# Kernel optimization log

Measured on AMD Instinct MI355X. Metric: run time of the kernel, lower is better.

The kernel has to match this reference:

```python
import jax, jax.numpy as jnp
import numpy as np

B, T, I, H, L = 64, 512, 512, 512, 2

def _xavier(key, shape):
    fan_in, fan_out = shape
    limit = float(np.sqrt(6.0 / (fan_in + fan_out)))
    return jax.random.uniform(key, shape, jnp.float32, -limit, limit)

def setup_inputs() -> dict:
    key = jax.random.key(0)
    ks = jax.random.split(key, 16)
    x = jax.random.normal(ks[0], (B, T, I), jnp.float32)
    h = jax.random.normal(ks[1], (L, B, H), jnp.float32)
    c = jax.random.normal(ks[2], (L, B, H), jnp.float32)
    # Gate order: i, f, g, o (concatenated along output dim -> [*, 4H])
    W_x0 = jnp.concatenate([_xavier(ks[3 + j], (I, H)) for j in range(4)], axis=1)
    W_h0 = jnp.concatenate([_xavier(ks[7 + j], (H, H)) for j in range(4)], axis=1)
    W_x1 = jnp.concatenate([_xavier(ks[11], (H, H)), _xavier(ks[12], (H, H)),
                            _xavier(ks[13], (H, H)), _xavier(ks[14], (H, H))], axis=1)
    W_h1 = jnp.concatenate([jax.random.split(ks[15], 4)[j] is None or _xavier(jax.random.split(ks[15], 4)[j], (H, H)) for j in range(4)], axis=1)
    # 8 scalar biases per layer: (b_ii, b_hi, b_if, b_hf, b_ig, b_hg, b_io, b_ho); zero-init as in torch
    b0 = jnp.zeros((8,), jnp.float32)
    b1 = jnp.zeros((8,), jnp.float32)
    return {"x": x, "h": h, "c": c, "W_x0": W_x0, "W_h0": W_h0, "b0": b0,
            "W_x1": W_x1, "W_h1": W_h1, "b1": b1}

def _lstm_layer(xs, h0, c0, Wx, Wh, b):
    # xs: [B, T, D]; Wx: [D, 4H]; Wh: [H, 4H]; b: [8] scalars
    bg = b[0::2] + b[1::2]  # combined per-gate scalar biases [4]: i, f, g, o
    x_proj = jnp.einsum('btd,dk->btk', xs, Wx)  # precompute input GEMM: [B, T, 4H]

    def step(carry, xp_t):
        h, c = carry
        z = xp_t + h @ Wh  # [B, 4H]
        zi, zf, zg, zo = jnp.split(z, 4, axis=1)
        i = jax.nn.sigmoid(zi + bg[0])
        f = jax.nn.sigmoid(zf + bg[1])
        g = jnp.tanh(zg + bg[2])
        o = jax.nn.sigmoid(zo + bg[3])
        c_new = f * c + i * g
        h_new = o * jnp.tanh(c_new)
        return (h_new, c_new), h_new

    (hT, cT), ys = jax.lax.scan(step, (h0, c0), jnp.swapaxes(x_proj, 0, 1))
    return jnp.swapaxes(ys, 0, 1), hT, cT  # output [B, T, H]

def reference(x, h, c, W_x0, W_h0, b0, W_x1, W_h1, b1):
    out0, h0T, c0T = _lstm_layer(x, h[0], c[0], W_x0, W_h0, b0)
    out1, h1T, c1T = _lstm_layer(out0, h[1], c[1], W_x1, W_h1, b1)
    new_h = jnp.stack([h0T, h1T])  # [L, B, H]
    new_c = jnp.stack([c0T, c1T])
    return out1, new_h, new_c
```

## Files before the change

### kernel.cpp

```cpp
#include <hip/hip_runtime.h>
#include <hip/hip_bf16.h>

#define B_   64
#define T_   512
#define I_   512
#define H_   512
#define NBLK 128
#define NTHR 256

typedef short bf16x8 __attribute__((ext_vector_type(8)));
typedef float f32x4  __attribute__((ext_vector_type(4)));
typedef unsigned long long u64;
typedef unsigned short u16;

#define MFMA(a, b, c) __builtin_amdgcn_mfma_f32_16x16x32_bf16((a), (b), (c), 0, 0, 0)

__device__ __forceinline__ u16 f2b(float f) {
    __hip_bfloat16 h = __float2bfloat16(f);
    return __builtin_bit_cast(u16, h);
}

__device__ __forceinline__ bf16x8 coh_ld8(const u16* p) {
    u64 lo = __hip_atomic_load((const u64*)p,     __ATOMIC_RELAXED, __HIP_MEMORY_SCOPE_AGENT);
    u64 hi = __hip_atomic_load((const u64*)p + 1, __ATOMIC_RELAXED, __HIP_MEMORY_SCOPE_AGENT);
    union { u64 q[2]; bf16x8 v; } u;
    u.q[0] = lo; u.q[1] = hi;
    return u.v;
}

__device__ __forceinline__ bool flag_ge(const int* f, int idx, int tgt) {
    return __hip_atomic_load(f + idx, __ATOMIC_RELAXED, __HIP_MEMORY_SCOPE_AGENT) >= tgt;
}

__global__ void k_init(const float* __restrict__ x, const float* __restrict__ h,
                       u16* __restrict__ xb, u16* __restrict__ h0ring, u16* __restrict__ h1ring,
                       int* __restrict__ flags0, int* __restrict__ flags1) {
    long i = (long)blockIdx.x * 256 + threadIdx.x;
    if (i < 2097152) {
        const float* p = x + i * 8;
        float4 a = *(const float4*)p;
        float4 b = *(const float4*)(p + 4);
        union { u16 s[8]; bf16x8 v; } u;
        u.s[0]=f2b(a.x); u.s[1]=f2b(a.y); u.s[2]=f2b(a.z); u.s[3]=f2b(a.w);
        u.s[4]=f2b(b.x); u.s[5]=f2b(b.y); u.s[6]=f2b(b.z); u.s[7]=f2b(b.w);
        *(bf16x8*)(xb + i * 8) = u.v;
    } else if (i < 2097152 + 8192) {
        long j = i - 2097152;
        const float* p = h + j * 8;
        #pragma unroll
        for (int jj = 0; jj < 8; ++jj) {
            long idx = j * 8 + jj;
            u16 v = f2b(p[jj]);
            if (idx < 32768) h0ring[7 * 32768 + idx] = v;
            else             h1ring[7 * 32768 + (idx - 32768)] = v;
        }
    } else if (i < 2097152 + 8192 + 512) {
        int j = (int)(i - (2097152 + 8192));
        if (j < 256) flags0[j] = 0; else flags1[j - 256] = 0;
    }
}

__global__ __launch_bounds__(NTHR, 1) void k_lstm(
    const u16* __restrict__ xb,
    const float* __restrict__ Wx0, const float* __restrict__ Wh0, const float* __restrict__ b0,
    const float* __restrict__ Wx1, const float* __restrict__ Wh1, const float* __restrict__ b1,
    const float* __restrict__ c_in,
    u16* __restrict__ h0ring, u16* __restrict__ h1ring,
    int* __restrict__ flags0, int* __restrict__ flags1,
    float* __restrict__ cs,
    float* __restrict__ out)
{
    const int tid  = threadIdx.x;
    const int bid  = blockIdx.x;
    const int lay  = bid >> 6;
    const int g    = (bid >> 4) & 3;
    const int u    = bid & 15;
    const int wave = tid >> 6;
    const int lane = tid & 63;
    const int n    = lane & 15;
    const int quad = lane >> 4;
    const int R0   = g * 16;
    const int U0   = u * 32;

    __shared__ __align__(16) u16   hstage[2][16][520];
    __shared__ __align__(16) u16   sc_hb[4][16][8];
    __shared__ __align__(16) float sc_h [4][16][8];

    const float* Wx = lay ? Wx1 : Wx0;
    const float* Wh = lay ? Wh1 : Wh0;
    const float* bb = lay ? b1  : b0;
    const float bi = bb[0] + bb[1];
    const float bf = bb[2] + bb[3];
    const float bg = bb[4] + bb[5];
    const float bo = bb[6] + bb[7];

    bf16x8 breg[2][32];
    #pragma unroll
    for (int ct = 0; ct < 2; ++ct) {
        const int gate = ct * 2 + (n >> 3);
        const int gcol = gate * 512 + U0 + wave * 8 + (n & 7);
        #pragma unroll
        for (int f = 0; f < 32; ++f) {
            const int kbase = f * 32 + quad * 8;
            bf16x8 w;
            #pragma unroll
            for (int j = 0; j < 8; ++j) {
                const int k = kbase + j;
                const float v = (k < 512) ? Wx[(size_t)k * 2048 + gcol]
                                          : Wh[(size_t)(k - 512) * 2048 + gcol];
                w[j] = (short)f2b(v);
            }
            breg[ct][f] = w;
        }
    }

    int* myflag = (lay ? flags1 : flags0) + g * 16 + u;
    const int fidx = g * 16 + n;
    (void)cs;

    float creg[4];
    if (n < 8) {
        #pragma unroll
        for (int r = 0; r < 4; ++r)
            creg[r] = c_in[(size_t)lay * 32768
                           + (size_t)(R0 + quad * 4 + r) * 512 + U0 + wave * 8 + n];
    }

    const int sr  = tid & 15;
    const int sch = tid >> 4;

    for (int t = 0; t < 512; ++t) {
        f32x4 acc0 = {0.f, 0.f, 0.f, 0.f};
        f32x4 acc1 = {0.f, 0.f, 0.f, 0.f};

        if (lay == 0) {
            const u16* px = xb + ((size_t)(R0 + n) * T_ + t) * I_;
            bf16x8 xa[16];
            #pragma unroll
            for (int f = 0; f < 16; ++f) xa[f] = *(const bf16x8*)(px + f * 32 + quad * 8);
            #pragma unroll
            for (int f = 0; f < 16; ++f) {
                acc0 = MFMA(xa[f], breg[0][f], acc0);
                acc1 = MFMA(xa[f], breg[1][f], acc1);
            }
            const bool bp = (t & 3) == 0;
            for (;;) {
                bool ok = flag_ge(flags0, fidx, t);
                if (bp) ok = ok && flag_ge(flags1, fidx, t - 4);
                if (__all(ok)) break;
                __builtin_amdgcn_s_sleep(1);
            }
            asm volatile("" ::: "memory");
            const u16* src = h0ring + (size_t)((t - 1) & 7) * 32768
                             + (size_t)(R0 + sr) * 512 + sch * 32;
            bf16x8 v0 = coh_ld8(src);
            bf16x8 v1 = coh_ld8(src + 8);
            bf16x8 v2 = coh_ld8(src + 16);
            bf16x8 v3 = coh_ld8(src + 24);
            *(bf16x8*)&hstage[0][sr][sch * 32]      = v0;
            *(bf16x8*)&hstage[0][sr][sch * 32 + 8]  = v1;
            *(bf16x8*)&hstage[0][sr][sch * 32 + 16] = v2;
            *(bf16x8*)&hstage[0][sr][sch * 32 + 24] = v3;
            __syncthreads();
            #pragma unroll
            for (int f = 0; f < 16; ++f) {
                bf16x8 ha = *(const bf16x8*)&hstage[0][n][f * 32 + quad * 8];
                acc0 = MFMA(ha, breg[0][16 + f], acc0);
                acc1 = MFMA(ha, breg[1][16 + f], acc1);
            }
        } else {
            for (;;) {
                bool ok = flag_ge(flags1, fidx, t) && flag_ge(flags0, fidx, t + 1);
                if (__all(ok)) break;
                __builtin_amdgcn_s_sleep(1);
            }
            asm volatile("" ::: "memory");
            const u16* s0 = h0ring + (size_t)(t & 7) * 32768
                            + (size_t)(R0 + sr) * 512 + sch * 32;
            const u16* s1 = h1ring + (size_t)((t - 1) & 7) * 32768
                            + (size_t)(R0 + sr) * 512 + sch * 32;
            bf16x8 a0 = coh_ld8(s0);
            bf16x8 a1 = coh_ld8(s0 + 8);
            bf16x8 a2 = coh_ld8(s0 + 16);
            bf16x8 a3 = coh_ld8(s0 + 24);
            bf16x8 b0v = coh_ld8(s1);
            bf16x8 b1v = coh_ld8(s1 + 8);
            bf16x8 b2v = coh_ld8(s1 + 16);
            bf16x8 b3v = coh_ld8(s1 + 24);
            *(bf16x8*)&hstage[0][sr][sch * 32]      = a0;
            *(bf16x8*)&hstage[0][sr][sch * 32 + 8]  = a1;
            *(bf16x8*)&hstage[0][sr][sch * 32 + 16] = a2;
            *(bf16x8*)&hstage[0][sr][sch * 32 + 24] = a3;
            *(bf16x8*)&hstage[1][sr][sch * 32]      = b0v;
            *(bf16x8*)&hstage[1][sr][sch * 32 + 8]  = b1v;
            *(bf16x8*)&hstage[1][sr][sch * 32 + 16] = b2v;
            *(bf16x8*)&hstage[1][sr][sch * 32 + 24] = b3v;
            __syncthreads();
            #pragma unroll
            for (int f = 0; f < 16; ++f) {
                bf16x8 ha = *(const bf16x8*)&hstage[0][n][f * 32 + quad * 8];
                acc0 = MFMA(ha, breg[0][f], acc0);
                acc1 = MFMA(ha, breg[1][f], acc1);
            }
            #pragma unroll
            for (int f = 0; f < 16; ++f) {
                bf16x8 ha = *(const bf16x8*)&hstage[1][n][f * 32 + quad * 8];
                acc0 = MFMA(ha, breg[0][16 + f], acc0);
                acc1 = MFMA(ha, breg[1][16 + f], acc1);
            }
        }

        f32x4 x0, x1;
        #pragma unroll
        for (int r = 0; r < 4; ++r) {
            x0[r] = __shfl_xor(acc0[r], 8);
            x1[r] = __shfl_xor(acc1[r], 8);
        }
        if (n < 8) {
            #pragma unroll
            for (int r = 0; r < 4; ++r) {
                const int row = quad * 4 + r;
                const float zi = acc0[r] + bi;
                const float zf = x0[r]   + bf;
                const float zg = acc1[r] + bg;
                const float zo = x1[r]   + bo;
                const float ig = 1.f / (1.f + __expf(-zi));
                const float fg = 1.f / (1.f + __expf(-zf));
                const float gg = tanhf(zg);
                const float og = 1.f / (1.f + __expf(-zo));
                const float cn = fg * creg[r] + ig * gg;
                const float hn = og * tanhf(cn);
                creg[r] = cn;
                sc_hb[wave][row][n] = f2b(hn);
                sc_h [wave][row][n] = hn;
            }
        }
        asm volatile("s_waitcnt lgkmcnt(0)" ::: "memory");

        if (lane < 16) {
            const u64* s = (const u64*)&sc_hb[wave][lane][0];
            u64 q0 = s[0], q1 = s[1];
            u64* d = (u64*)((lay ? h1ring : h0ring) + (size_t)(t & 7) * 32768
                            + (size_t)(R0 + lane) * 512 + U0 + wave * 8);
            __hip_atomic_store(d,     q0, __ATOMIC_RELAXED, __HIP_MEMORY_SCOPE_AGENT);
            __hip_atomic_store(d + 1, q1, __ATOMIC_RELAXED, __HIP_MEMORY_SCOPE_AGENT);
        }
        asm volatile("s_waitcnt vmcnt(0)" ::: "memory");
        __syncthreads();
        if (tid == 0)
            __hip_atomic_store(myflag, t + 1, __ATOMIC_RELAXED, __HIP_MEMORY_SCOPE_AGENT);

        if (lay && lane < 16) {
            const float* s = &sc_h[wave][lane][0];
            f32x4 a  = *(const f32x4*)s;
            f32x4 b2 = *(const f32x4*)(s + 4);
            float* po = out + ((size_t)(R0 + lane) * T_ + t) * H_ + U0 + wave * 8;
            *(f32x4*)po       = a;
            *(f32x4*)(po + 4) = b2;
        }
        if (t == 511 && n < 8) {
            const size_t o1 = (size_t)B_ * T_ * H_;
            #pragma unroll
            for (int r = 0; r < 4; ++r) {
                const int grow = R0 + quad * 4 + r;
                out[o1 +         (size_t)lay * 32768 + (size_t)grow * 512 + U0 + wave * 8 + n]
                    = sc_h[wave][quad * 4 + r][n];
                out[o1 + 65536 + (size_t)lay * 32768 + (size_t)grow * 512 + U0 + wave * 8 + n]
                    = creg[r];
            }
        }
    }
}

extern "C" void kernel_launch(void* const* d_in, const int* in_sizes, int n_in,
                              void* d_out, int out_size, void* d_ws, size_t ws_size,
                              hipStream_t stream) {
    const float* x   = (const float*)d_in[0];
    const float* h   = (const float*)d_in[1];
    const float* c   = (const float*)d_in[2];
    const float* Wx0 = (const float*)d_in[3];
    const float* Wh0 = (const float*)d_in[4];
    const float* b0  = (const float*)d_in[5];
    const float* Wx1 = (const float*)d_in[6];
    const float* Wh1 = (const float*)d_in[7];
    const float* b1  = (const float*)d_in[8];
    float* out = (float*)d_out;

    u16* xb     = (u16*)d_ws;
    u16* h0ring = xb + 16777216;
    u16* h1ring = h0ring + 262144;
    int* flags0 = (int*)(h1ring + 262144);
    int* flags1 = flags0 + 256;
    float* cs   = (float*)(flags1 + 256);

    k_init<<<8226, 256, 0, stream>>>(x, h, xb, h0ring, h1ring, flags0, flags1);
    k_lstm<<<NBLK, NTHR, 0, stream>>>(xb, Wx0, Wh0, b0, Wx1, Wh1, b1, c,
                                      h0ring, h1ring, flags0, flags1, cs, out);
}
```

Before: 3.588 ms.

## Coalesce h ring loads, swizzle LDS staging, and single-wave publish of h

Replaces the per-thread 4x16-byte strided loads of the previous hidden state with fully coalesced 8-byte atomic loads, where consecutive threads read consecutive words of a row. The data is stored into an XOR-swizzled LDS layout to avoid bank conflicts. The layer-1 loops interleave the two h sources. The h writeback is restructured so wave 0 alone stores the whole 16x32 tile contiguously and then raises the flag, which drops one barrier-wait path but serialises publishing onto one wave.

```diff
diff --git a/kernel.cpp b/kernel.cpp
--- a/kernel.cpp
+++ b/kernel.cpp
@@ -20,12 +20,11 @@
     return __builtin_bit_cast(u16, h);
 }
 
-__device__ __forceinline__ bf16x8 coh_ld8(const u16* p) {
-    u64 lo = __hip_atomic_load((const u64*)p,     __ATOMIC_RELAXED, __HIP_MEMORY_SCOPE_AGENT);
-    u64 hi = __hip_atomic_load((const u64*)p + 1, __ATOMIC_RELAXED, __HIP_MEMORY_SCOPE_AGENT);
-    union { u64 q[2]; bf16x8 v; } u;
-    u.q[0] = lo; u.q[1] = hi;
-    return u.v;
+__device__ __forceinline__ u64 coh_ld64(const void* p) {
+    return __hip_atomic_load((const u64*)p, __ATOMIC_RELAXED, __HIP_MEMORY_SCOPE_AGENT);
+}
+__device__ __forceinline__ void coh_st64(void* p, u64 v) {
+    __hip_atomic_store((u64*)p, v, __ATOMIC_RELAXED, __HIP_MEMORY_SCOPE_AGENT);
 }
 
 __device__ __forceinline__ bool flag_ge(const int* f, int idx, int tgt) {
@@ -82,8 +81,8 @@
     const int R0   = g * 16;
     const int U0   = u * 32;
 
-    __shared__ __align__(16) u16   hstage[2][16][520];
-    __shared__ __align__(16) u16   sc_hb[4][16][8];
+    __shared__ __align__(16) u16   hstage[2][8192];
+    __shared__ __align__(16) u16   sc_all[16 * 36];
     __shared__ __align__(16) float sc_h [4][16][8];
 
     const float* Wx = lay ? Wx1 : Wx0;
@@ -126,9 +125,6 @@
                            + (size_t)(R0 + quad * 4 + r) * 512 + U0 + wave * 8 + n];
     }
 
-    const int sr  = tid & 15;
-    const int sch = tid >> 4;
-
     for (int t = 0; t < 512; ++t) {
         f32x4 acc0 = {0.f, 0.f, 0.f, 0.f};
         f32x4 acc1 = {0.f, 0.f, 0.f, 0.f};
@@ -151,20 +147,26 @@
                 __builtin_amdgcn_s_sleep(1);
             }
             asm volatile("" ::: "memory");
-            const u16* src = h0ring + (size_t)((t - 1) & 7) * 32768
-                             + (size_t)(R0 + sr) * 512 + sch * 32;
-            bf16x8 v0 = coh_ld8(src);
-            bf16x8 v1 = coh_ld8(src + 8);
-            bf16x8 v2 = coh_ld8(src + 16);
-            bf16x8 v3 = coh_ld8(src + 24);
-            *(bf16x8*)&hstage[0][sr][sch * 32]      = v0;
-            *(bf16x8*)&hstage[0][sr][sch * 32 + 8]  = v1;
-            *(bf16x8*)&hstage[0][sr][sch * 32 + 16] = v2;
-            *(bf16x8*)&hstage[0][sr][sch * 32 + 24] = v3;
+            const u16* base = h0ring + (size_t)((t - 1) & 7) * 32768;
+            u64 v[8];
+            #pragma unroll
+            for (int i = 0; i < 8; ++i) {
+                const int s = i * 256 + tid;
+                const int r = s >> 7, m = s & 127;
+                v[i] = coh_ld64(base + (size_t)(R0 + r) * 512 + m * 4);
+            }
+            #pragma unroll
+            for (int i = 0; i < 8; ++i) {
+                const int s = i * 256 + tid;
+                const int r = s >> 7, m = s & 127;
+                const int uu = m >> 1, sub = m & 1;
+                *(u64*)&hstage[0][r * 512 + (((uu ^ (r & 7)) << 3) | (sub << 2))] = v[i];
+            }
             __syncthreads();
             #pragma unroll
             for (int f = 0; f < 16; ++f) {
-                bf16x8 ha = *(const bf16x8*)&hstage[0][n][f * 32 + quad * 8];
+                bf16x8 ha = *(const bf16x8*)
+                    &hstage[0][n * 512 + (((f * 4 + quad) ^ (n & 7)) << 3)];
                 acc0 = MFMA(ha, breg[0][16 + f], acc0);
                 acc1 = MFMA(ha, breg[1][16 + f], acc1);
             }
@@ -175,38 +177,35 @@
                 __builtin_amdgcn_s_sleep(1);
             }
             asm volatile("" ::: "memory");
-            const u16* s0 = h0ring + (size_t)(t & 7) * 32768
-                            + (size_t)(R0 + sr) * 512 + sch * 32;
-            const u16* s1 = h1ring + (size_t)((t - 1) & 7) * 32768
-                            + (size_t)(R0 + sr) * 512 + sch * 32;
-            bf16x8 a0 = coh_ld8(s0);
-            bf16x8 a1 = coh_ld8(s0 + 8);
-            bf16x8 a2 = coh_ld8(s0 + 16);
-            bf16x8 a3 = coh_ld8(s0 + 24);
-            bf16x8 b0v = coh_ld8(s1);
-            bf16x8 b1v = coh_ld8(s1 + 8);
-            bf16x8 b2v = coh_ld8(s1 + 16);
-            bf16x8 b3v = coh_ld8(s1 + 24);
-            *(bf16x8*)&hstage[0][sr][sch * 32]      = a0;
-            *(bf16x8*)&hstage[0][sr][sch * 32 + 8]  = a1;
-            *(bf16x8*)&hstage[0][sr][sch * 32 + 16] = a2;
-            *(bf16x8*)&hstage[0][sr][sch * 32 + 24] = a3;
-            *(bf16x8*)&hstage[1][sr][sch * 32]      = b0v;
-            *(bf16x8*)&hstage[1][sr][sch * 32 + 8]  = b1v;
-            *(bf16x8*)&hstage[1][sr][sch * 32 + 16] = b2v;
-            *(bf16x8*)&hstage[1][sr][sch * 32 + 24] = b3v;
+            const u16* base0 = h0ring + (size_t)(t & 7) * 32768;
+            const u16* base1 = h1ring + (size_t)((t - 1) & 7) * 32768;
+            u64 v0[8], v1[8];
+            #pragma unroll
+            for (int i = 0; i < 8; ++i) {
+                const int s = i * 256 + tid;
+                const int r = s >> 7, m = s & 127;
+                v0[i] = coh_ld64(base0 + (size_t)(R0 + r) * 512 + m * 4);
+                v1[i] = coh_ld64(base1 + (size_t)(R0 + r) * 512 + m * 4);
+            }
+            #pragma unroll
+            for (int i = 0; i < 8; ++i) {
+                const int s = i * 256 + tid;
+                const int r = s >> 7, m = s & 127;
+                const int uu = m >> 1, sub = m & 1;
+                const int off = r * 512 + (((uu ^ (r & 7)) << 3) | (sub << 2));
+                *(u64*)&hstage[0][off] = v0[i];
+                *(u64*)&hstage[1][off] = v1[i];
+            }
             __syncthreads();
             #pragma unroll
             for (int f = 0; f < 16; ++f) {
-                bf16x8 ha = *(const bf16x8*)&hstage[0][n][f * 32 + quad * 8];
+                const int off = n * 512 + (((f * 4 + quad) ^ (n & 7)) << 3);
+                bf16x8 ha = *(const bf16x8*)&hstage[0][off];
                 acc0 = MFMA(ha, breg[0][f], acc0);
                 acc1 = MFMA(ha, breg[1][f], acc1);
-            }
-            #pragma unroll
-            for (int f = 0; f < 16; ++f) {
-                bf16x8 ha = *(const bf16x8*)&hstage[1][n][f * 32 + quad * 8];
-                acc0 = MFMA(ha, breg[0][16 + f], acc0);
-                acc1 = MFMA(ha, breg[1][16 + f], acc1);
+                bf16x8 hb = *(const bf16x8*)&hstage[1][off];
+                acc0 = MFMA(hb, breg[0][16 + f], acc0);
+                acc1 = MFMA(hb, breg[1][16 + f], acc1);
             }
         }
 
@@ -231,24 +230,25 @@
                 const float cn = fg * creg[r] + ig * gg;
                 const float hn = og * tanhf(cn);
                 creg[r] = cn;
-                sc_hb[wave][row][n] = f2b(hn);
+                sc_all[row * 36 + wave * 8 + n] = f2b(hn);
                 sc_h [wave][row][n] = hn;
             }
         }
-        asm volatile("s_waitcnt lgkmcnt(0)" ::: "memory");
-
-        if (lane < 16) {
-            const u64* s = (const u64*)&sc_hb[wave][lane][0];
-            u64 q0 = s[0], q1 = s[1];
-            u64* d = (u64*)((lay ? h1ring : h0ring) + (size_t)(t & 7) * 32768
-                            + (size_t)(R0 + lane) * 512 + U0 + wave * 8);
-            __hip_atomic_store(d,     q0, __ATOMIC_RELAXED, __HIP_MEMORY_SCOPE_AGENT);
-            __hip_atomic_store(d + 1, q1, __ATOMIC_RELAXED, __HIP_MEMORY_SCOPE_AGENT);
-        }
-        asm volatile("s_waitcnt vmcnt(0)" ::: "memory");
         __syncthreads();
-        if (tid == 0)
-            __hip_atomic_store(myflag, t + 1, __ATOMIC_RELAXED, __HIP_MEMORY_SCOPE_AGENT);
+
+        if (wave == 0) {
+            u16* ring = (lay ? h1ring : h0ring) + (size_t)(t & 7) * 32768;
+            #pragma unroll
+            for (int k = 0; k < 2; ++k) {
+                const int j   = k * 64 + lane;
+                const int row = j >> 3, s8 = j & 7;
+                u64 vv = *(const u64*)&sc_all[row * 36 + s8 * 4];
+                coh_st64(ring + (size_t)(R0 + row) * 512 + U0 + s8 * 4, vv);
+            }
+            asm volatile("s_waitcnt vmcnt(0)" ::: "memory");
+            if (lane == 0)
+                __hip_atomic_store(myflag, t + 1, __ATOMIC_RELAXED, __HIP_MEMORY_SCOPE_AGENT);
+        }
 
         if (lay && lane < 16) {
             const float* s = &sc_h[wave][lane][0];
```

Result: faster. 3.138 ms (-12.5%).
